# Kernel tuning notes

Hardware: AMD Instinct MI355X
Metric: run time of the kernel (lower is better)

The kernel has to match this reference:

```python
import jax, jax.numpy as jnp
import numpy as np

N_CLUSTERS = 512
TEMPERATURE = 0.1


def setup_inputs() -> dict:
    key = jax.random.key(0)
    k1, k2 = jax.random.split(key)
    x = jax.random.normal(k1, (32, 1024, 256), dtype=jnp.float32)
    centroids = jax.random.normal(k2, (N_CLUSTERS, 256), dtype=jnp.float32)
    return {"x": x, "centroids": centroids}


def reference(x, centroids):
    # Flatten non-cluster axes into a sample axis: [N, D]
    B, S, D = x.shape
    xf = x.reshape(-1, D)  # [N, D]
    x_sq = jnp.sum(xf * xf, axis=-1, keepdims=True)           # [N, 1]
    c_sq = jnp.sum(centroids * centroids, axis=-1)             # [K]
    cross = jnp.einsum('nd,kd->nk', xf, centroids)             # [N, K]
    dists = x_sq - 2.0 * cross + c_sq[None, :]                 # [N, K]
    # Temperature-scaled soft assignments
    assignments = jax.nn.softmax(-dists / TEMPERATURE, axis=-1)  # [N, K]
    # Restore leading (non-feature) dims, append cluster axis
    return assignments.reshape(B, S, N_CLUSTERS)
```

## Files before the change

### kernel.cpp

```cpp
#include <hip/hip_runtime.h>

#define NROWS 32768
#define KC 512
#define DDIM 256
#define BM 64
#define BK 32
#define KCH (DDIM / BK)
#define CHUNK_USH (KC * BK)

typedef __attribute__((ext_vector_type(8))) short bf16x8;
typedef __attribute__((ext_vector_type(4))) float f32x4;

union U8 { unsigned short u[8]; bf16x8 v; };

__device__ __forceinline__ unsigned short f2bf(float f) {
    union { float f; unsigned int u; } a; a.f = f;
    unsigned int r = a.u + 0x7fffu + ((a.u >> 16) & 1u);
    return (unsigned short)(r >> 16);
}
__device__ __forceinline__ float bf2f(unsigned short h) {
    union { unsigned int u; float f; } a; a.u = ((unsigned int)h) << 16;
    return a.f;
}
__device__ __forceinline__ void ld16(const void* g, void* l) {
    __builtin_amdgcn_global_load_lds(
        (const __attribute__((address_space(1))) unsigned int*)g,
        (__attribute__((address_space(3))) unsigned int*)l, 16, 0, 0);
}

__global__ __launch_bounds__(64) void prep_c(const float* __restrict__ c,
                                             unsigned short* __restrict__ bhi,
                                             unsigned short* __restrict__ blo,
                                             float* __restrict__ csq10) {
    const int n = blockIdx.x, lane = threadIdx.x;
    const int d0 = lane * 4;
    float4 v = ((const float4*)(c + (size_t)n * DDIM))[lane];
    float vv[4] = {v.x, v.y, v.z, v.w};
    unsigned short hh[4], ll[4];
    float ssq = 0.f;
    #pragma unroll
    for (int i = 0; i < 4; ++i) {
        ssq += vv[i] * vv[i];
        hh[i] = f2bf(vv[i]);
        ll[i] = f2bf(vv[i] - bf2f(hh[i]));
    }
    #pragma unroll
    for (int off = 32; off; off >>= 1) ssq += __shfl_xor(ssq, off);
    if (lane == 0) csq10[n] = 10.f * ssq;
    const int ks = d0 >> 5;
    const int q  = (d0 >> 3) & 3;
    const int s  = q ^ ((n >> 1) & 3);
    const size_t dst = (size_t)ks * CHUNK_USH + (n * 4 + s) * 8 + (d0 & 7);
    *(ushort4*)(bhi + dst) = make_ushort4(hh[0], hh[1], hh[2], hh[3]);
    *(ushort4*)(blo + dst) = make_ushort4(ll[0], ll[1], ll[2], ll[3]);
}

union SmemU {
    struct { unsigned short Bh[CHUNK_USH], Bl[CHUNK_USH]; } k;
    float lbuf[16 * 516];
};

__global__ __launch_bounds__(512, 4) void kmeans_mfma(
    const float* __restrict__ x, const unsigned short* __restrict__ bhi,
    const unsigned short* __restrict__ blo, const float* __restrict__ csq10,
    float* __restrict__ out) {
    __shared__ __align__(16) SmemU sm;
    __shared__ float red[2][4][BM];

    const int tid  = threadIdx.x;
    const int w    = tid >> 6, lane = tid & 63;
    const int wm   = w >> 2, wn = w & 3;
    const int cc   = lane & 15, q = lane >> 4;
    const int row0 = blockIdx.x * BM;

    f32x4 acc[2][8];
    #pragma unroll
    for (int mt = 0; mt < 2; ++mt)
        #pragma unroll
        for (int t = 0; t < 8; ++t) acc[mt][t] = (f32x4){0.f, 0.f, 0.f, 0.f};

    const float* xA0 = x + (size_t)(row0 + wm * 32 + cc) * DDIM + q * 8;
    const float* xA1 = xA0 + (size_t)16 * DDIM;
    const int sF = q ^ ((cc >> 1) & 3);
    const int bF = (4 * cc + sF) * 8;
    const int dmaOff = w * 2048;

    const int s0 = ((blockIdx.x >> 3) & 1) * 4;

    {
        const size_t cb = (size_t)s0 * CHUNK_USH;
        #pragma unroll
        for (int j = 0; j < 4; ++j) {
            const int o = dmaOff + j * 512;
            ld16(bhi + cb + o + lane * 8, &sm.k.Bh[o]);
            ld16(blo + cb + o + lane * 8, &sm.k.Bl[o]);
        }
    }
    const int k0 = s0 * BK;
    float4 c00 = *(const float4*)(xA0 + k0);
    float4 c01 = *(const float4*)(xA0 + k0 + 4);
    float4 c10 = *(const float4*)(xA1 + k0);
    float4 c11 = *(const float4*)(xA1 + k0 + 4);
    __syncthreads();

    for (int i = 0; i < KCH; ++i) {
        const int nks = (s0 + i + 1) & (KCH - 1);
        float4 n00, n01, n10, n11;
        if (i < KCH - 1) {
            const int kn = nks * BK;
            n00 = *(const float4*)(xA0 + kn);
            n01 = *(const float4*)(xA0 + kn + 4);
            n10 = *(const float4*)(xA1 + kn);
            n11 = *(const float4*)(xA1 + kn + 4);
        }
        bf16x8 ah[2], al[2];
        {
            float v0[8] = {c00.x, c00.y, c00.z, c00.w, c01.x, c01.y, c01.z, c01.w};
            float v1[8] = {c10.x, c10.y, c10.z, c10.w, c11.x, c11.y, c11.z, c11.w};
            U8 H0, L0, H1, L1;
            #pragma unroll
            for (int e = 0; e < 8; ++e) {
                H0.u[e] = f2bf(v0[e]); L0.u[e] = f2bf(v0[e] - bf2f(H0.u[e]));
                H1.u[e] = f2bf(v1[e]); L1.u[e] = f2bf(v1[e] - bf2f(H1.u[e]));
            }
            ah[0] = H0.v; al[0] = L0.v; ah[1] = H1.v; al[1] = L1.v;
        }
        #pragma unroll
        for (int t = 0; t < 8; ++t) {
            const int bo = (wn * 8 + t) * 512 + bF;
            bf16x8 bh = *(const bf16x8*)&sm.k.Bh[bo];
            bf16x8 bl = *(const bf16x8*)&sm.k.Bl[bo];
            acc[0][t] = __builtin_amdgcn_mfma_f32_16x16x32_bf16(ah[0], bh, acc[0][t], 0, 0, 0);
            acc[1][t] = __builtin_amdgcn_mfma_f32_16x16x32_bf16(ah[1], bh, acc[1][t], 0, 0, 0);
            acc[0][t] = __builtin_amdgcn_mfma_f32_16x16x32_bf16(ah[0], bl, acc[0][t], 0, 0, 0);
            acc[1][t] = __builtin_amdgcn_mfma_f32_16x16x32_bf16(ah[1], bl, acc[1][t], 0, 0, 0);
            acc[0][t] = __builtin_amdgcn_mfma_f32_16x16x32_bf16(al[0], bh, acc[0][t], 0, 0, 0);
            acc[1][t] = __builtin_amdgcn_mfma_f32_16x16x32_bf16(al[1], bh, acc[1][t], 0, 0, 0);
        }
        __syncthreads();
        if (i < KCH - 1) {
            const size_t cb = (size_t)nks * CHUNK_USH;
            #pragma unroll
            for (int j = 0; j < 4; ++j) {
                const int o = dmaOff + j * 512;
                ld16(bhi + cb + o + lane * 8, &sm.k.Bh[o]);
                ld16(blo + cb + o + lane * 8, &sm.k.Bl[o]);
            }
            __syncthreads();
        }
        c00 = n00; c01 = n01; c10 = n10; c11 = n11;
    }

    float csqv[8];
    #pragma unroll
    for (int t = 0; t < 8; ++t) csqv[t] = csq10[wn * 128 + t * 16 + cc];
    const int rb = wm * 32 + q * 4;
    float M[2][4], I[2][4];
    #pragma unroll
    for (int mt = 0; mt < 2; ++mt)
        #pragma unroll
        for (int g = 0; g < 4; ++g) {
            float pm = -1e30f;
            #pragma unroll
            for (int t = 0; t < 8; ++t) pm = fmaxf(pm, 20.f * acc[mt][t][g] - csqv[t]);
            #pragma unroll
            for (int off = 1; off < 16; off <<= 1) pm = fmaxf(pm, __shfl_xor(pm, off));
            if (cc == 0) red[0][wn][rb + mt * 16 + g] = pm;
        }
    __syncthreads();
    #pragma unroll
    for (int mt = 0; mt < 2; ++mt)
        #pragma unroll
        for (int g = 0; g < 4; ++g) {
            const int ri = rb + mt * 16 + g;
            const float m = fmaxf(fmaxf(red[0][0][ri], red[0][1][ri]),
                                  fmaxf(red[0][2][ri], red[0][3][ri]));
            M[mt][g] = m;
            float ps = 0.f;
            #pragma unroll
            for (int t = 0; t < 8; ++t) ps += __expf(20.f * acc[mt][t][g] - csqv[t] - m);
            #pragma unroll
            for (int off = 1; off < 16; off <<= 1) ps += __shfl_xor(ps, off);
            if (cc == 0) red[1][wn][ri] = ps;
        }
    __syncthreads();
    #pragma unroll
    for (int mt = 0; mt < 2; ++mt)
        #pragma unroll
        for (int g = 0; g < 4; ++g) {
            const int ri = rb + mt * 16 + g;
            I[mt][g] = 1.f / (red[1][0][ri] + red[1][1][ri] +
                              red[1][2][ri] + red[1][3][ri]);
        }

    #pragma unroll
    for (int p = 0; p < 4; ++p) {
        if (wm == (p >> 1)) {
            const int mt = p & 1;
            #pragma unroll
            for (int g = 0; g < 4; ++g) {
                const int   lr = q * 4 + g;
                const float mg = M[mt][g], ig = I[mt][g];
                #pragma unroll
                for (int t = 0; t < 8; ++t)
                    sm.lbuf[lr * 516 + wn * 128 + t * 16 + cc] =
                        __expf(20.f * acc[mt][t][g] - csqv[t] - mg) * ig;
            }
        }
        __syncthreads();
        #pragma unroll
        for (int j = 0; j < 4; ++j) {
            const int f    = j * 512 + tid;
            const int lrow = f >> 7;
            const int c4   = f & 127;
            float4    v    = *(const float4*)&sm.lbuf[lrow * 516 + c4 * 4];
            *(float4*)(out + (size_t)(row0 + p * 16 + lrow) * KC + c4 * 4) = v;
        }
        __syncthreads();
    }
}

extern "C" void kernel_launch(void* const* d_in, const int* in_sizes, int n_in,
                              void* d_out, int out_size, void* d_ws, size_t ws_size,
                              hipStream_t stream) {
    const float* x   = (const float*)d_in[0];
    const float* c   = (const float*)d_in[1];
    float*       out = (float*)d_out;

    unsigned short* bhi   = (unsigned short*)d_ws;
    unsigned short* blo   = bhi + (size_t)KCH * CHUNK_USH;
    float*          csq10 = (float*)(blo + (size_t)KCH * CHUNK_USH);

    prep_c<<<KC, 64, 0, stream>>>(c, bhi, blo, csq10);
    kmeans_mfma<<<NROWS / BM, 512, 0, stream>>>(x, bhi, blo, csq10, out);
}
```

Before: 122.8 us.

## Double-buffer centroid hi/lo tiles and overlap DMA with MFMA

Reorganizes the centroid bf16 hi/lo tables into a linear per-fragment layout without the XOR swizzle, so each lane reads a contiguous 16 bytes. The main loop now ping-pongs between two LDS buffers: while MFMAs consume the hi half, the lo half is loaded into the other buffer, and vice versa. This is meant to hide global-to-LDS load latency behind matrix math. It also drops the staggered starting k-chunk per block and the software-prefetched x registers, so x loads are now issued just before use, and concurrent blocks contend for the same B chunk.

New measurement: 126.2 us. 2.7% more time.

```diff
diff --git a/kernel.cpp b/kernel.cpp
--- a/kernel.cpp
+++ b/kernel.cpp
@@ -49,14 +49,14 @@
     if (lane == 0) csq10[n] = 10.f * ssq;
     const int ks = d0 >> 5;
     const int q  = (d0 >> 3) & 3;
-    const int s  = q ^ ((n >> 1) & 3);
-    const size_t dst = (size_t)ks * CHUNK_USH + (n * 4 + s) * 8 + (d0 & 7);
+    const int t  = n >> 4, cc = n & 15;
+    const size_t dst = ((size_t)ks * CHUNK_USH) + ((size_t)t * 64 + (q * 16 + cc)) * 8 + (d0 & 7);
     *(ushort4*)(bhi + dst) = make_ushort4(hh[0], hh[1], hh[2], hh[3]);
     *(ushort4*)(blo + dst) = make_ushort4(ll[0], ll[1], ll[2], ll[3]);
 }
 
 union SmemU {
-    struct { unsigned short Bh[CHUNK_USH], Bl[CHUNK_USH]; } k;
+    unsigned short tab[2][CHUNK_USH];
     float lbuf[16 * 516];
 };
 
@@ -81,37 +81,29 @@
 
     const float* xA0 = x + (size_t)(row0 + wm * 32 + cc) * DDIM + q * 8;
     const float* xA1 = xA0 + (size_t)16 * DDIM;
-    const int sF = q ^ ((cc >> 1) & 3);
-    const int bF = (4 * cc + sF) * 8;
-    const int dmaOff = w * 2048;
-
-    const int s0 = ((blockIdx.x >> 3) & 1) * 4;
-
-    {
-        const size_t cb = (size_t)s0 * CHUNK_USH;
-        #pragma unroll
-        for (int j = 0; j < 4; ++j) {
-            const int o = dmaOff + j * 512;
-            ld16(bhi + cb + o + lane * 8, &sm.k.Bh[o]);
-            ld16(blo + cb + o + lane * 8, &sm.k.Bl[o]);
-        }
-    }
-    const int k0 = s0 * BK;
-    float4 c00 = *(const float4*)(xA0 + k0);
-    float4 c01 = *(const float4*)(xA0 + k0 + 4);
-    float4 c10 = *(const float4*)(xA1 + k0);
-    float4 c11 = *(const float4*)(xA1 + k0 + 4);
+    const int dmaOff = w * 4 * 512;
+    const int rdOff = (wn * 8) * 512 + lane * 8;
+
+    float4 c00 = *(const float4*)xA0;
+    float4 c01 = *(const float4*)(xA0 + 4);
+    float4 c10 = *(const float4*)xA1;
+    float4 c11 = *(const float4*)(xA1 + 4);
+    #pragma unroll
+    for (int j = 0; j < 4; ++j) {
+        const int o = dmaOff + j * 512;
+        ld16(bhi + o + lane * 8, &sm.tab[0][o]);
+    }
     __syncthreads();
 
-    for (int i = 0; i < KCH; ++i) {
-        const int nks = (s0 + i + 1) & (KCH - 1);
-        float4 n00, n01, n10, n11;
-        if (i < KCH - 1) {
-            const int kn = nks * BK;
-            n00 = *(const float4*)(xA0 + kn);
-            n01 = *(const float4*)(xA0 + kn + 4);
-            n10 = *(const float4*)(xA1 + kn);
-            n11 = *(const float4*)(xA1 + kn + 4);
+    int cur = 0;
+    for (int ks = 0; ks < KCH; ++ks) {
+        {
+            const unsigned short* src = blo + (size_t)ks * CHUNK_USH;
+            #pragma unroll
+            for (int j = 0; j < 4; ++j) {
+                const int o = dmaOff + j * 512;
+                ld16(src + o + lane * 8, &sm.tab[cur ^ 1][o]);
+            }
         }
         bf16x8 ah[2], al[2];
         {
@@ -127,28 +119,36 @@
         }
         #pragma unroll
         for (int t = 0; t < 8; ++t) {
-            const int bo = (wn * 8 + t) * 512 + bF;
-            bf16x8 bh = *(const bf16x8*)&sm.k.Bh[bo];
-            bf16x8 bl = *(const bf16x8*)&sm.k.Bl[bo];
+            bf16x8 bh = *(const bf16x8*)&sm.tab[cur][rdOff + t * 512];
             acc[0][t] = __builtin_amdgcn_mfma_f32_16x16x32_bf16(ah[0], bh, acc[0][t], 0, 0, 0);
             acc[1][t] = __builtin_amdgcn_mfma_f32_16x16x32_bf16(ah[1], bh, acc[1][t], 0, 0, 0);
+            acc[0][t] = __builtin_amdgcn_mfma_f32_16x16x32_bf16(al[0], bh, acc[0][t], 0, 0, 0);
+            acc[1][t] = __builtin_amdgcn_mfma_f32_16x16x32_bf16(al[1], bh, acc[1][t], 0, 0, 0);
+        }
+        __syncthreads();
+        cur ^= 1;
+
+        if (ks < KCH - 1) {
+            const int kn = (ks + 1) * BK;
+            c00 = *(const float4*)(xA0 + kn);
+            c01 = *(const float4*)(xA0 + kn + 4);
+            c10 = *(const float4*)(xA1 + kn);
+            c11 = *(const float4*)(xA1 + kn + 4);
+            const unsigned short* src = bhi + (size_t)(ks + 1) * CHUNK_USH;
+            #pragma unroll
+            for (int j = 0; j < 4; ++j) {
+                const int o = dmaOff + j * 512;
+                ld16(src + o + lane * 8, &sm.tab[cur ^ 1][o]);
+            }
+        }
+        #pragma unroll
+        for (int t = 0; t < 8; ++t) {
+            bf16x8 bl = *(const bf16x8*)&sm.tab[cur][rdOff + t * 512];
             acc[0][t] = __builtin_amdgcn_mfma_f32_16x16x32_bf16(ah[0], bl, acc[0][t], 0, 0, 0);
             acc[1][t] = __builtin_amdgcn_mfma_f32_16x16x32_bf16(ah[1], bl, acc[1][t], 0, 0, 0);
-            acc[0][t] = __builtin_amdgcn_mfma_f32_16x16x32_bf16(al[0], bh, acc[0][t], 0, 0, 0);
-            acc[1][t] = __builtin_amdgcn_mfma_f32_16x16x32_bf16(al[1], bh, acc[1][t], 0, 0, 0);
-        }
-        __syncthreads();
-        if (i < KCH - 1) {
-            const size_t cb = (size_t)nks * CHUNK_USH;
-            #pragma unroll
-            for (int j = 0; j < 4; ++j) {
-                const int o = dmaOff + j * 512;
-                ld16(bhi + cb + o + lane * 8, &sm.k.Bh[o]);
-                ld16(blo + cb + o + lane * 8, &sm.k.Bl[o]);
-            }
-            __syncthreads();
-        }
-        c00 = n00; c01 = n01; c10 = n10; c11 = n11;
+        }
+        __syncthreads();
+        cur ^= 1;
     }
 
     float csqv[8];
```
